# Kernel optimization log

Hardware: AMD Instinct MI355X
Metric: run time of the kernel (lower is better)

## Reference

```python
import jax, jax.numpy as jnp
import numpy as np


def setup_inputs() -> dict:
    key = jax.random.key(0)
    k1, k2 = jax.random.split(key)
    B, Lc, Lm, D = 8, 2048, 2048, 128
    context = jax.random.normal(k1, (B, Lc, D), dtype=jnp.float32)
    main = jax.random.normal(k2, (B, Lm, D), dtype=jnp.float32)
    return {"context": context, "main": main}


def reference(context, main):
    # weights[b,c,m] = sum_d context[b,c,d] * main[b,m,d]   (Keras dot axes=[2,2])
    weights = jnp.einsum("bcd,bmd->bcm", context, main)
    # K.softmax default axis=-1: normalize over the main-length axis m
    weights = jax.nn.softmax(weights, axis=-1)
    # dot([weights, context], axes=1): contract axis 1 (c) of both -> (B, Lm, D)
    weighted = jnp.einsum("bcm,bcd->bmd", weights, context)
    return main - weighted
```

## Files before the change

### kernel.cpp

```cpp
#include <hip/hip_runtime.h>


#define BATCH 8
#define L_SEQ 2048
#define DD 128
#define SHIFT 40.0f
#define LDA 136

typedef __attribute__((ext_vector_type(8))) short bf16x8;
typedef __attribute__((ext_vector_type(4))) short bf16x4;
typedef __attribute__((ext_vector_type(4))) float f32x4;

__device__ __forceinline__ short f2bf(float f) {
    unsigned u = __builtin_bit_cast(unsigned, f);
    return (short)((u + 0x8000u) >> 16);
}

__device__ __forceinline__ void gl2lds16(const short* g, short* l) {
    __builtin_amdgcn_global_load_lds(
        (const __attribute__((address_space(1))) unsigned int*)g,
        (__attribute__((address_space(3))) unsigned int*)l, 16, 0, 0);
}

template <int NT>
__device__ __forceinline__ void stage_tile(short* __restrict__ dst,
                                           const float* __restrict__ src,
                                           int nelts, int t) {
    for (int base = 0; base < nelts; base += NT * 8) {
        int flat = base + t * 8;
        const float4* p = (const float4*)(src + flat);
        float4 v0 = p[0];
        float4 v1 = p[1];
        bf16x8 s;
        s[0] = f2bf(v0.x); s[1] = f2bf(v0.y); s[2] = f2bf(v0.z); s[3] = f2bf(v0.w);
        s[4] = f2bf(v1.x); s[5] = f2bf(v1.y); s[6] = f2bf(v1.z); s[7] = f2bf(v1.w);
        int row = flat >> 7;
        int col = flat & 127;
        *(bf16x8*)&dst[row * LDA + col] = s;
    }
}

__global__ __launch_bounds__(256) void zero_kernel(float* __restrict__ p, int n) {
    int i = blockIdx.x * 256 + threadIdx.x;
    if (i < n) p[i] = 0.0f;
}


__global__ __launch_bounds__(256) void convert_kernel(const float* __restrict__ ctx,
                                                      const float* __restrict__ mn,
                                                      short* __restrict__ Cbf,
                                                      short* __restrict__ Mbf,
                                                      float* __restrict__ Lg) {
    int tid = blockIdx.x * 256 + threadIdx.x;
    if (tid < BATCH * L_SEQ) Lg[tid] = 0.0f;
    const int half = BATCH * L_SEQ * DD / 8;
    int id = tid;
    const float* src;
    short* dst;
    if (id < half) { src = ctx; dst = Cbf; }
    else           { id -= half; src = mn; dst = Mbf; }
    int row = id >> 4;
    int lc = id & 15;
    const float4* p = (const float4*)(src + ((size_t)row << 7) + lc * 8);
    float4 v0 = p[0];
    float4 v1 = p[1];
    bf16x8 s;
    s[0] = f2bf(v0.x); s[1] = f2bf(v0.y); s[2] = f2bf(v0.z); s[3] = f2bf(v0.w);
    s[4] = f2bf(v1.x); s[5] = f2bf(v1.y); s[6] = f2bf(v1.z); s[7] = f2bf(v1.w);
    int pc = (lc & 8) | ((lc ^ row) & 7);
    *(bf16x8*)&dst[((size_t)row << 7) + pc * 8] = s;
}

__global__ __launch_bounds__(256, 2) void stats_kernel(const short* __restrict__ Cbf,
                                                       const short* __restrict__ Mbf,
                                                       float* __restrict__ Lg,
                                                       short* __restrict__ Eg) {
    __shared__ short Cs[128 * 128];
    __shared__ short Ms[2][64 * 128];

    int bid = blockIdx.x;
    int mc = bid & 3;
    int ct = (bid >> 2) & 15;
    int b  = bid >> 6;
    int t = threadIdx.x;
    int w = t >> 6;
    int l = t & 63;
    int a15 = l & 15;
    int q = l >> 4;
    int h = a15 & 7;
    int cw = (w & 1) * 64;
    int mw = (w >> 1) * 32;

    {
        const short* gC = Cbf + ((size_t)(b * L_SEQ + ct * 128)) * DD;
        const short* gM = Mbf + ((size_t)(b * L_SEQ + mc * 512)) * DD;
        #pragma unroll
        for (int ii = 0; ii < 8; ++ii) {
            int inst = w * 8 + ii;
            gl2lds16(gC + inst * 512 + l * 8, Cs + inst * 512);
        }
        #pragma unroll
        for (int ii = 0; ii < 4; ++ii) {
            int inst = w * 4 + ii;
            gl2lds16(gM + inst * 512 + l * 8, Ms[0] + inst * 512);
        }
    }

    __syncthreads();

    {
        const short* gM = Mbf + ((size_t)(b * L_SEQ + mc * 512 + 64)) * DD;
        #pragma unroll
        for (int ii = 0; ii < 4; ++ii) {
            int inst = w * 4 + ii;
            gl2lds16(gM + inst * 512 + l * 8, Ms[1] + inst * 512);
        }
    }

    bf16x8 af[4][4];
    #pragma unroll
    for (int ks = 0; ks < 4; ++ks) {
        int aoff = ((ks * 4 + q) ^ h) * 8;
        #pragma unroll
        for (int i = 0; i < 4; ++i)
            af[ks][i] = *(const bf16x8*)&Cs[(cw + i * 16 + a15) * 128 + aoff];
    }

    float ls[4][4] = {};

    for (int ms = 0; ms < 8; ++ms) {
        int bp = ms & 1;
        if (ms > 0) {
            __syncthreads();
            if (ms < 7) {
                const short* gM = Mbf + ((size_t)(b * L_SEQ + mc * 512 + (ms + 1) * 64)) * DD;
                #pragma unroll
                for (int ii = 0; ii < 4; ++ii) {
                    int inst = w * 4 + ii;
                    gl2lds16(gM + inst * 512 + l * 8, Ms[bp ^ 1] + inst * 512);
                }
            }
        }

        f32x4 acc[4][2];
        #pragma unroll
        for (int i = 0; i < 4; ++i)
            #pragma unroll
            for (int j = 0; j < 2; ++j) {
                f32x4 z = {0.f, 0.f, 0.f, 0.f};
                acc[i][j] = z;
            }
        #pragma unroll
        for (int ks = 0; ks < 4; ++ks) {
            int aoff = ((ks * 4 + q) ^ h) * 8;
            bf16x8 bv[2];
            #pragma unroll
            for (int j = 0; j < 2; ++j)
                bv[j] = *(const bf16x8*)&Ms[bp][(mw + j * 16 + a15) * 128 + aoff];
            #pragma unroll
            for (int i = 0; i < 4; ++i)
                #pragma unroll
                for (int j = 0; j < 2; ++j)
                    acc[i][j] = __builtin_amdgcn_mfma_f32_16x16x32_bf16(af[ks][i], bv[j], acc[i][j], 0, 0, 0);
        }

        #pragma unroll
        for (int j = 0; j < 2; ++j) {
            int m = mc * 512 + ms * 64 + mw + j * 16 + a15;
            size_t rowb = ((size_t)(b * L_SEQ + m)) * L_SEQ;
            #pragma unroll
            for (int i = 0; i < 4; ++i) {
                bf16x4 pk;
                #pragma unroll
                for (int r = 0; r < 4; ++r) {
                    float e = __expf(acc[i][j][r] - SHIFT);
                    ls[i][r] += e;
                    pk[r] = f2bf(e);
                }
                int cq = ct * 128 + cw + i * 16 + q * 4;
                int chunk = cq >> 3;
                int pcc = (chunk & ~7) | ((chunk ^ m) & 7);
                *(bf16x4*)&Eg[rowb + pcc * 8 + (cq & 7)] = pk;
            }
        }
    }

    #pragma unroll
    for (int i = 0; i < 4; ++i)
        #pragma unroll
        for (int r = 0; r < 4; ++r) {
            float v = ls[i][r];
            v += __shfl_xor(v, 1);
            v += __shfl_xor(v, 2);
            v += __shfl_xor(v, 4);
            v += __shfl_xor(v, 8);
            ls[i][r] = v;
        }
    if (a15 == 0) {
        #pragma unroll
        for (int i = 0; i < 4; ++i) {
            int c = ct * 128 + cw + i * 16 + q * 4;
            #pragma unroll
            for (int r = 0; r < 4; ++r)
                atomicAdd(&Lg[(size_t)b * L_SEQ + c + r], ls[i][r]);
        }
    }
}

__global__ __launch_bounds__(256) void prep_kernel(const float* __restrict__ ctx,
                                                   const float* __restrict__ Lg,
                                                   short* __restrict__ CtL) {
    __shared__ short Ts[128 * LDA];
    __shared__ float invLs[128];

    int b = blockIdx.x >> 4;
    int cc = blockIdx.x & 15;
    int t = threadIdx.x;

    if (t < 128) invLs[t] = 1.0f / Lg[(size_t)b * L_SEQ + cc * 128 + t];
    __syncthreads();

    const float* src = ctx + ((size_t)(b * L_SEQ + cc * 128)) * DD;
    #pragma unroll
    for (int i = 0; i < 8; ++i) {
        int flat = i * 2048 + t * 8;
        int r = flat >> 7;
        int c = flat & 127;
        const float4* p = (const float4*)(src + flat);
        float4 v0 = p[0];
        float4 v1 = p[1];
        float il = invLs[r];
        bf16x8 s;
        s[0] = f2bf(v0.x * il); s[1] = f2bf(v0.y * il); s[2] = f2bf(v0.z * il); s[3] = f2bf(v0.w * il);
        s[4] = f2bf(v1.x * il); s[5] = f2bf(v1.y * il); s[6] = f2bf(v1.z * il); s[7] = f2bf(v1.w * il);
        *(bf16x8*)&Ts[r * LDA + c] = s;
    }
    __syncthreads();

    int d = t >> 1;
    int ch = (t & 1) * 64;
    int key = d & 7;
    #pragma unroll
    for (int i = 0; i < 8; ++i) {
        int c = ch + i * 8;
        bf16x8 v;
        #pragma unroll
        for (int j = 0; j < 8; ++j) v[j] = Ts[(c + j) * LDA + d];
        int pc = cc * 16 + (ch >> 3) + (i ^ key);
        *(bf16x8*)&CtL[((size_t)(b * DD + d)) * L_SEQ + pc * 8] = v;
    }
}

__global__ __launch_bounds__(256, 2) void attend_kernel(const short* __restrict__ Eg,
                                                        const short* __restrict__ CtL,
                                                        const float* __restrict__ mn,
                                                        float* __restrict__ out) {
    __shared__ short Et2[2][32 * 128];
    __shared__ short Ct2[2][128 * 128];

    int bid = blockIdx.x;
    int mtile = bid & 63;
    int b = bid >> 6;
    int m0 = mtile * 32;
    int t = threadIdx.x;
    int w = t >> 6;
    int l = t & 63;
    int a15 = l & 15;
    int q = l >> 4;
    int h = a15 & 7;
    int lcc = l & 15;

    f32x4 acc[2][2] = {{{0.f,0.f,0.f,0.f},{0.f,0.f,0.f,0.f}},
                       {{0.f,0.f,0.f,0.f},{0.f,0.f,0.f,0.f}}};

    #pragma unroll
    for (int ii = 0; ii < 2; ++ii) {
        int inst = w * 2 + ii;
        gl2lds16(Eg + ((size_t)(b * L_SEQ + m0 + inst * 4 + q)) * L_SEQ + lcc * 8,
                 &Et2[0][inst * 512]);
    }
    #pragma unroll
    for (int ii = 0; ii < 8; ++ii) {
        int inst = w * 8 + ii;
        gl2lds16(CtL + ((size_t)(b * DD + inst * 4 + q)) * L_SEQ + lcc * 8,
                 &Ct2[0][inst * 512]);
    }

    for (int cs = 0; cs < 16; ++cs) {
        int bp = cs & 1;
        __syncthreads();

        if (cs < 15) {
            int c0 = (cs + 1) * 128;
            #pragma unroll
            for (int ii = 0; ii < 2; ++ii) {
                int inst = w * 2 + ii;
                gl2lds16(Eg + ((size_t)(b * L_SEQ + m0 + inst * 4 + q)) * L_SEQ + c0 + lcc * 8,
                         &Et2[bp ^ 1][inst * 512]);
            }
            #pragma unroll
            for (int ii = 0; ii < 8; ++ii) {
                int inst = w * 8 + ii;
                gl2lds16(CtL + ((size_t)(b * DD + inst * 4 + q)) * L_SEQ + c0 + lcc * 8,
                         &Ct2[bp ^ 1][inst * 512]);
            }
        }

        const short* EtB = Et2[bp];
        const short* CtB = Ct2[bp];
        #pragma unroll
        for (int ks = 0; ks < 4; ++ks) {
            int aoff = ((ks * 4 + q) ^ h) * 8;
            bf16x8 a0 = *(const bf16x8*)&EtB[a15 * 128 + aoff];
            bf16x8 a1 = *(const bf16x8*)&EtB[(16 + a15) * 128 + aoff];
            bf16x8 b0 = *(const bf16x8*)&CtB[((w * 2 + 0) * 16 + a15) * 128 + aoff];
            bf16x8 b1 = *(const bf16x8*)&CtB[((w * 2 + 1) * 16 + a15) * 128 + aoff];
            acc[0][0] = __builtin_amdgcn_mfma_f32_16x16x32_bf16(a0, b0, acc[0][0], 0, 0, 0);
            acc[0][1] = __builtin_amdgcn_mfma_f32_16x16x32_bf16(a0, b1, acc[0][1], 0, 0, 0);
            acc[1][0] = __builtin_amdgcn_mfma_f32_16x16x32_bf16(a1, b0, acc[1][0], 0, 0, 0);
            acc[1][1] = __builtin_amdgcn_mfma_f32_16x16x32_bf16(a1, b1, acc[1][1], 0, 0, 0);
        }
    }

    #pragma unroll
    for (int mg = 0; mg < 2; ++mg) {
        #pragma unroll
        for (int g = 0; g < 2; ++g) {
            int d = (w * 2 + g) * 16 + a15;
            #pragma unroll
            for (int r = 0; r < 4; ++r) {
                int m = m0 + mg * 16 + q * 4 + r;
                size_t idx = ((size_t)(b * L_SEQ + m)) * DD + d;
                out[idx] = mn[idx] - acc[mg][g][r];
            }
        }
    }
}


__global__ __launch_bounds__(256, 4) void stats_fb(const float* __restrict__ ctx,
                                                   const float* __restrict__ mn,
                                                   float* __restrict__ Lg) {
    __shared__ short Cs[64 * LDA];
    __shared__ short Ms[64 * LDA];

    int bid = blockIdx.x;
    int mc = bid & 3;
    int ct = (bid >> 2) & 31;
    int b  = bid >> 7;
    int t = threadIdx.x;
    int w = t >> 6;
    int l = t & 63;
    int a15 = l & 15;
    int q = l >> 4;

    stage_tile<256>(Cs, ctx + ((size_t)b * L_SEQ + ct * 64) * DD, 64 * DD, t);

    float ls[4] = {0.f, 0.f, 0.f, 0.f};
    for (int mt = 0; mt < 8; ++mt) {
        __syncthreads();
        int m0 = (mc * 8 + mt) * 64;
        stage_tile<256>(Ms, mn + ((size_t)b * L_SEQ + m0) * DD, 64 * DD, t);
        __syncthreads();

        f32x4 acc[4] = {{0.f,0.f,0.f,0.f},{0.f,0.f,0.f,0.f},{0.f,0.f,0.f,0.f},{0.f,0.f,0.f,0.f}};
        #pragma unroll
        for (int ks = 0; ks < 4; ++ks) {
            int k0 = ks * 32 + q * 8;
            bf16x8 a = *(const bf16x8*)&Cs[(w * 16 + a15) * LDA + k0];
            #pragma unroll
            for (int g = 0; g < 4; ++g) {
                bf16x8 bb = *(const bf16x8*)&Ms[(g * 16 + a15) * LDA + k0];
                acc[g] = __builtin_amdgcn_mfma_f32_16x16x32_bf16(a, bb, acc[g], 0, 0, 0);
            }
        }
        #pragma unroll
        for (int g = 0; g < 4; ++g)
            #pragma unroll
            for (int r = 0; r < 4; ++r)
                ls[r] += __expf(acc[g][r] - SHIFT);
    }

    #pragma unroll
    for (int r = 0; r < 4; ++r) {
        float v = ls[r];
        v += __shfl_xor(v, 1);
        v += __shfl_xor(v, 2);
        v += __shfl_xor(v, 4);
        v += __shfl_xor(v, 8);
        ls[r] = v;
    }
    if (a15 == 0) {
        int c = ct * 64 + w * 16 + q * 4;
        #pragma unroll
        for (int r = 0; r < 4; ++r)
            atomicAdd(&Lg[(size_t)b * L_SEQ + c + r], ls[r]);
    }
}

__global__ __launch_bounds__(1024, 4) void attend_fb(const float* __restrict__ ctx,
                                                     const float* __restrict__ mn,
                                                     const float* __restrict__ Lg,
                                                     float* __restrict__ out) {
    __shared__ short Mt[64 * LDA];
    __shared__ short Cs[128 * LDA];
    __shared__ short Ct[128 * LDA];
    __shared__ short Ps[64 * LDA];
    __shared__ float invLs[128];

    int bid = blockIdx.x;
    int mtile = bid & 31;
    int b = bid >> 5;
    int m0 = mtile * 64;
    int t = threadIdx.x;
    int w = t >> 6;
    int l = t & 63;
    int a15 = l & 15;
    int q = l >> 4;
    int mg = w & 3;
    int pg = w >> 2;

    stage_tile<1024>(Mt, mn + ((size_t)b * L_SEQ + m0) * DD, 64 * DD, t);

    f32x4 oacc[2] = {{0.f,0.f,0.f,0.f},{0.f,0.f,0.f,0.f}};

    for (int cs = 0; cs < 16; ++cs) {
        int c0 = cs * 128;
        __syncthreads();
        stage_tile<1024>(Cs, ctx + ((size_t)b * L_SEQ + c0) * DD, 128 * DD, t);
        if (t < 128) invLs[t] = 1.0f / Lg[(size_t)b * L_SEQ + c0 + t];
        __syncthreads();

        {
            int cc = t & 127;
            int d0 = (t >> 7) * 16;
            #pragma unroll
            for (int hh = 0; hh < 2; ++hh) {
                bf16x8 v = *(const bf16x8*)&Cs[cc * LDA + d0 + hh * 8];
                #pragma unroll
                for (int j = 0; j < 8; ++j)
                    Ct[(d0 + hh * 8 + j) * LDA + cc] = v[j];
            }
        }

        f32x4 sacc[2] = {{0.f,0.f,0.f,0.f},{0.f,0.f,0.f,0.f}};
        #pragma unroll
        for (int ks = 0; ks < 4; ++ks) {
            int k0 = ks * 32 + q * 8;
            bf16x8 a = *(const bf16x8*)&Mt[(mg * 16 + a15) * LDA + k0];
            #pragma unroll
            for (int g = 0; g < 2; ++g) {
                bf16x8 bb = *(const bf16x8*)&Cs[((pg * 2 + g) * 16 + a15) * LDA + k0];
                sacc[g] = __builtin_amdgcn_mfma_f32_16x16x32_bf16(a, bb, sacc[g], 0, 0, 0);
            }
        }
        #pragma unroll
        for (int g = 0; g < 2; ++g) {
            int cl = (pg * 2 + g) * 16 + a15;
            float il = invLs[cl];
            #pragma unroll
            for (int r = 0; r < 4; ++r) {
                float p = __expf(sacc[g][r] - SHIFT) * il;
                Ps[(mg * 16 + q * 4 + r) * LDA + cl] = f2bf(p);
            }
        }
        __syncthreads();

        #pragma unroll
        for (int ks = 0; ks < 4; ++ks) {
            int k0 = ks * 32 + q * 8;
            bf16x8 a = *(const bf16x8*)&Ps[(mg * 16 + a15) * LDA + k0];
            #pragma unroll
            for (int g = 0; g < 2; ++g) {
                bf16x8 bb = *(const bf16x8*)&Ct[((pg * 2 + g) * 16 + a15) * LDA + k0];
                oacc[g] = __builtin_amdgcn_mfma_f32_16x16x32_bf16(a, bb, oacc[g], 0, 0, 0);
            }
        }
    }

    #pragma unroll
    for (int g = 0; g < 2; ++g) {
        int dl = (pg * 2 + g) * 16 + a15;
        #pragma unroll
        for (int r = 0; r < 4; ++r) {
            int ml = mg * 16 + q * 4 + r;
            size_t idx = ((size_t)b * L_SEQ + m0 + ml) * DD + dl;
            out[idx] = mn[idx] - oacc[g][r];
        }
    }
}


extern "C" void kernel_launch(void* const* d_in, const int* in_sizes, int n_in,
                              void* d_out, int out_size, void* d_ws, size_t ws_size,
                              hipStream_t stream) {
    const float* ctx = (const float*)d_in[0];
    const float* mn  = (const float*)d_in[1];
    float* out = (float*)d_out;

    const size_t LG_BYTES = (size_t)BATCH * L_SEQ * sizeof(float);
    const size_t BF_BYTES = (size_t)BATCH * L_SEQ * DD * sizeof(short);
    const size_t E_BYTES  = (size_t)BATCH * L_SEQ * L_SEQ * sizeof(short);
    const size_t NEED = LG_BYTES + 3 * BF_BYTES + E_BYTES;

    float* Lg = (float*)d_ws;

    if (ws_size >= NEED) {
        short* Cbf = (short*)((char*)d_ws + LG_BYTES);
        short* Mbf = (short*)((char*)d_ws + LG_BYTES + BF_BYTES);
        short* CtL = (short*)((char*)d_ws + LG_BYTES + 2 * BF_BYTES);
        short* Eg  = (short*)((char*)d_ws + LG_BYTES + 3 * BF_BYTES);
        convert_kernel<<<2048, 256, 0, stream>>>(ctx, mn, Cbf, Mbf, Lg);
        stats_kernel<<<BATCH * 16 * 4, 256, 0, stream>>>(Cbf, Mbf, Lg, Eg);
        prep_kernel<<<BATCH * 16, 256, 0, stream>>>(ctx, Lg, CtL);
        attend_kernel<<<BATCH * 64, 256, 0, stream>>>(Eg, CtL, mn, out);
    } else {
        int nL = BATCH * L_SEQ;
        zero_kernel<<<(nL + 255) / 256, 256, 0, stream>>>(Lg, nL);
        stats_fb<<<BATCH * 32 * 4, 256, 0, stream>>>(ctx, mn, Lg);
        attend_fb<<<BATCH * 32, 1024, 0, stream>>>(ctx, mn, Lg, out);
    }
}
```

Baseline: 114.5 us.

## Recompute exp scores in attend kernel instead of materializing E matrix

The stats kernel no longer writes the bf16 exponentiated score matrix (B×L×L) to global memory. A new fused attend kernel recomputes the context·main scores with 32x32 MFMAs, applies exp, repacks the results in registers via lane shuffles into A operands, and accumulates against the normalized transposed context. Partial outputs from the four c-split waves are reduced through LDS. This removes a 64MB write and read of E at the cost of recomputing the first GEMM.

After: 119.2 us. 1.04x slower.

```diff
diff --git a/kernel.cpp b/kernel.cpp
--- a/kernel.cpp
+++ b/kernel.cpp
@@ -10,6 +10,8 @@
 typedef __attribute__((ext_vector_type(8))) short bf16x8;
 typedef __attribute__((ext_vector_type(4))) short bf16x4;
 typedef __attribute__((ext_vector_type(4))) float f32x4;
+typedef __attribute__((ext_vector_type(16))) float f32x16;
+typedef __attribute__((ext_vector_type(4))) unsigned int uint4v;
 
 __device__ __forceinline__ short f2bf(float f) {
     unsigned u = __builtin_bit_cast(unsigned, f);
@@ -73,8 +75,7 @@
 
 __global__ __launch_bounds__(256, 2) void stats_kernel(const short* __restrict__ Cbf,
                                                        const short* __restrict__ Mbf,
-                                                       float* __restrict__ Lg,
-                                                       short* __restrict__ Eg) {
+                                                       float* __restrict__ Lg) {
     __shared__ short Cs[128 * 128];
     __shared__ short Ms[2][64 * 128];
 
@@ -165,24 +166,12 @@
         }
 
         #pragma unroll
-        for (int j = 0; j < 2; ++j) {
-            int m = mc * 512 + ms * 64 + mw + j * 16 + a15;
-            size_t rowb = ((size_t)(b * L_SEQ + m)) * L_SEQ;
-            #pragma unroll
-            for (int i = 0; i < 4; ++i) {
-                bf16x4 pk;
+        for (int j = 0; j < 2; ++j)
+            #pragma unroll
+            for (int i = 0; i < 4; ++i)
                 #pragma unroll
-                for (int r = 0; r < 4; ++r) {
-                    float e = __expf(acc[i][j][r] - SHIFT);
-                    ls[i][r] += e;
-                    pk[r] = f2bf(e);
-                }
-                int cq = ct * 128 + cw + i * 16 + q * 4;
-                int chunk = cq >> 3;
-                int pcc = (chunk & ~7) | ((chunk ^ m) & 7);
-                *(bf16x4*)&Eg[rowb + pcc * 8 + (cq & 7)] = pk;
-            }
-        }
+                for (int r = 0; r < 4; ++r)
+                    ls[i][r] += __expf(acc[i][j][r] - SHIFT);
     }
 
     #pragma unroll
@@ -251,88 +240,164 @@
     }
 }
 
-__global__ __launch_bounds__(256, 2) void attend_kernel(const short* __restrict__ Eg,
-                                                        const short* __restrict__ CtL,
-                                                        const float* __restrict__ mn,
-                                                        float* __restrict__ out) {
-    __shared__ short Et2[2][32 * 128];
-    __shared__ short Ct2[2][128 * 128];
+__global__ __launch_bounds__(512, 2) void attend_fused(const short* __restrict__ Cbf,
+                                                       const short* __restrict__ Mbf,
+                                                       const short* __restrict__ CtL,
+                                                       const float* __restrict__ mn,
+                                                       float* __restrict__ out) {
+    __shared__ __align__(16) char smem[131072];
 
     int bid = blockIdx.x;
-    int mtile = bid & 63;
-    int b = bid >> 6;
-    int m0 = mtile * 32;
+    int mtile = bid & 31;
+    int b = bid >> 5;
     int t = threadIdx.x;
     int w = t >> 6;
     int l = t & 63;
-    int a15 = l & 15;
-    int q = l >> 4;
-    int h = a15 & 7;
-    int lcc = l & 15;
-
-    f32x4 acc[2][2] = {{{0.f,0.f,0.f,0.f},{0.f,0.f,0.f,0.f}},
-                       {{0.f,0.f,0.f,0.f},{0.f,0.f,0.f,0.f}}};
-
-    #pragma unroll
-    for (int ii = 0; ii < 2; ++ii) {
-        int inst = w * 2 + ii;
-        gl2lds16(Eg + ((size_t)(b * L_SEQ + m0 + inst * 4 + q)) * L_SEQ + lcc * 8,
-                 &Et2[0][inst * 512]);
-    }
-    #pragma unroll
-    for (int ii = 0; ii < 8; ++ii) {
-        int inst = w * 8 + ii;
-        gl2lds16(CtL + ((size_t)(b * DD + inst * 4 + q)) * L_SEQ + lcc * 8,
-                 &Ct2[0][inst * 512]);
-    }
+    int la = l & 31;
+    int hi = l >> 5;
+    int mg = w >> 2;
+    int ch = w & 3;
+
+    int m_glob = mtile * 64 + mg * 32 + la;
+
+    bf16x8 mf[8];
+    {
+        const short* mrow = Mbf + ((size_t)(b * L_SEQ + m_glob)) * DD;
+        int key = m_glob & 7;
+        #pragma unroll
+        for (int ks = 0; ks < 8; ++ks) {
+            int lc = ks * 2 + hi;
+            int pc = (lc & 8) | ((lc ^ key) & 7);
+            mf[ks] = *(const bf16x8*)&mrow[pc * 8];
+        }
+    }
+
+    auto stage = [&](int cs, int p) {
+        short* Cw = (short*)(smem + p * 65536);
+        short* Tw = (short*)(smem + p * 65536 + 32768);
+        const short* gC = Cbf + ((size_t)(b * L_SEQ + cs * 128)) * DD;
+        #pragma unroll
+        for (int ii = 0; ii < 4; ++ii) {
+            int inst = w * 4 + ii;
+            gl2lds16(gC + inst * 512 + l * 8, Cw + inst * 512);
+        }
+        const short* gT = CtL + (size_t)b * DD * L_SEQ + (size_t)cs * 128;
+        #pragma unroll
+        for (int ii = 0; ii < 4; ++ii) {
+            int inst = w * 4 + ii;
+            int row = inst * 4 + (l >> 4);
+            gl2lds16(gT + (size_t)row * L_SEQ + (l & 15) * 8, Tw + inst * 512);
+        }
+    };
+
+    f32x16 o[4];
+    #pragma unroll
+    for (int dg = 0; dg < 4; ++dg)
+        #pragma unroll
+        for (int r = 0; r < 16; ++r) o[dg][r] = 0.0f;
+
+    stage(0, 0);
 
     for (int cs = 0; cs < 16; ++cs) {
-        int bp = cs & 1;
+        int p = cs & 1;
         __syncthreads();
-
-        if (cs < 15) {
-            int c0 = (cs + 1) * 128;
-            #pragma unroll
-            for (int ii = 0; ii < 2; ++ii) {
-                int inst = w * 2 + ii;
-                gl2lds16(Eg + ((size_t)(b * L_SEQ + m0 + inst * 4 + q)) * L_SEQ + c0 + lcc * 8,
-                         &Et2[bp ^ 1][inst * 512]);
-            }
-            #pragma unroll
-            for (int ii = 0; ii < 8; ++ii) {
-                int inst = w * 8 + ii;
-                gl2lds16(CtL + ((size_t)(b * DD + inst * 4 + q)) * L_SEQ + c0 + lcc * 8,
-                         &Ct2[bp ^ 1][inst * 512]);
-            }
-        }
-
-        const short* EtB = Et2[bp];
-        const short* CtB = Ct2[bp];
-        #pragma unroll
-        for (int ks = 0; ks < 4; ++ks) {
-            int aoff = ((ks * 4 + q) ^ h) * 8;
-            bf16x8 a0 = *(const bf16x8*)&EtB[a15 * 128 + aoff];
-            bf16x8 a1 = *(const bf16x8*)&EtB[(16 + a15) * 128 + aoff];
-            bf16x8 b0 = *(const bf16x8*)&CtB[((w * 2 + 0) * 16 + a15) * 128 + aoff];
-            bf16x8 b1 = *(const bf16x8*)&CtB[((w * 2 + 1) * 16 + a15) * 128 + aoff];
-            acc[0][0] = __builtin_amdgcn_mfma_f32_16x16x32_bf16(a0, b0, acc[0][0], 0, 0, 0);
-            acc[0][1] = __builtin_amdgcn_mfma_f32_16x16x32_bf16(a0, b1, acc[0][1], 0, 0, 0);
-            acc[1][0] = __builtin_amdgcn_mfma_f32_16x16x32_bf16(a1, b0, acc[1][0], 0, 0, 0);
-            acc[1][1] = __builtin_amdgcn_mfma_f32_16x16x32_bf16(a1, b1, acc[1][1], 0, 0, 0);
-        }
-    }
-
-    #pragma unroll
-    for (int mg = 0; mg < 2; ++mg) {
-        #pragma unroll
-        for (int g = 0; g < 2; ++g) {
-            int d = (w * 2 + g) * 16 + a15;
-            #pragma unroll
-            for (int r = 0; r < 4; ++r) {
-                int m = m0 + mg * 16 + q * 4 + r;
-                size_t idx = ((size_t)(b * L_SEQ + m)) * DD + d;
-                out[idx] = mn[idx] - acc[mg][g][r];
-            }
+        if (cs < 15) stage(cs + 1, p ^ 1);
+
+        const short* Cw = (const short*)(smem + p * 65536);
+        const short* Tw = (const short*)(smem + p * 65536 + 32768);
+
+        f32x16 s;
+        #pragma unroll
+        for (int r = 0; r < 16; ++r) s[r] = 0.0f;
+        int crow = ch * 32 + la;
+        int ckey = la & 7;
+        #pragma unroll
+        for (int ks = 0; ks < 8; ++ks) {
+            int lc = ks * 2 + hi;
+            int pc = (lc & 8) | ((lc ^ ckey) & 7);
+            bf16x8 av = *(const bf16x8*)&Cw[crow * 128 + pc * 8];
+            s = __builtin_amdgcn_mfma_f32_32x32x16_bf16(av, mf[ks], s, 0, 0, 0);
+        }
+
+        unsigned u[4][2];
+        #pragma unroll
+        for (int q = 0; q < 4; ++q)
+            #pragma unroll
+            for (int jj = 0; jj < 2; ++jj) {
+                float e0 = __expf(s[q * 4 + jj * 2]     - SHIFT);
+                float e1 = __expf(s[q * 4 + jj * 2 + 1] - SHIFT);
+                u[q][jj] = ((unsigned)(unsigned short)f2bf(e1) << 16)
+                         |  (unsigned)(unsigned short)f2bf(e0);
+            }
+
+        bf16x8 pa[2];
+        #pragma unroll
+        for (int ks2 = 0; ks2 < 2; ++ks2) {
+            unsigned a0 = u[2 * ks2][0],     a1 = u[2 * ks2][1];
+            unsigned b0 = u[2 * ks2 + 1][0], b1 = u[2 * ks2 + 1][1];
+            unsigned a0p = (unsigned)__shfl_xor((int)a0, 32);
+            unsigned a1p = (unsigned)__shfl_xor((int)a1, 32);
+            unsigned b0p = (unsigned)__shfl_xor((int)b0, 32);
+            unsigned b1p = (unsigned)__shfl_xor((int)b1, 32);
+            uint4v pw;
+            pw.x = hi ? b0p : a0;
+            pw.y = hi ? b1p : a1;
+            pw.z = hi ? b0  : a0p;
+            pw.w = hi ? b1  : a1p;
+            pa[ks2] = __builtin_bit_cast(bf16x8, pw);
+        }
+
+        #pragma unroll
+        for (int dg = 0; dg < 4; ++dg) {
+            int drow = dg * 32 + la;
+            int dkey = drow & 7;
+            #pragma unroll
+            for (int ks2 = 0; ks2 < 2; ++ks2) {
+                int lc2 = ch * 4 + ks2 * 2 + hi;
+                int pc2 = (lc2 & 8) | ((lc2 ^ dkey) & 7);
+                bf16x8 tv = *(const bf16x8*)&Tw[drow * 128 + pc2 * 8];
+                o[dg] = __builtin_amdgcn_mfma_f32_32x32x16_bf16(tv, pa[ks2], o[dg], 0, 0, 0);
+            }
+        }
+    }
+
+    __syncthreads();
+    float* red = (float*)smem;
+    {
+        float* base = red + w * 4096;
+        #pragma unroll
+        for (int dg = 0; dg < 4; ++dg)
+            #pragma unroll
+            for (int r = 0; r < 16; ++r) {
+                int d = dg * 32 + (r & 3) + 8 * (r >> 2) + 4 * hi;
+                base[d * 32 + la] = o[dg][r];
+            }
+    }
+    __syncthreads();
+
+    {
+        int mg2 = t >> 8;
+        int dq  = (t >> 5) & 7;
+        int m   = t & 31;
+        int m_out = mtile * 64 + mg2 * 32 + m;
+        size_t gbase = ((size_t)(b * L_SEQ + m_out)) * DD + dq * 16;
+        const float* r0 = red + (mg2 * 4 + 0) * 4096;
+        const float* r1 = red + (mg2 * 4 + 1) * 4096;
+        const float* r2 = red + (mg2 * 4 + 2) * 4096;
+        const float* r3 = red + (mg2 * 4 + 3) * 4096;
+        #pragma unroll
+        for (int jq = 0; jq < 4; ++jq) {
+            f32x4 v;
+            #pragma unroll
+            for (int e = 0; e < 4; ++e) {
+                int idx = (dq * 16 + jq * 4 + e) * 32 + m;
+                v[e] = r0[idx] + r1[idx] + r2[idx] + r3[idx];
+            }
+            f32x4 mv = *(const f32x4*)&mn[gbase + jq * 4];
+            f32x4 ov;
+            ov[0] = mv[0] - v[0]; ov[1] = mv[1] - v[1];
+            ov[2] = mv[2] - v[2]; ov[3] = mv[3] - v[3];
+            *(f32x4*)&out[gbase + jq * 4] = ov;
         }
     }
 }
@@ -500,8 +565,7 @@
 
     const size_t LG_BYTES = (size_t)BATCH * L_SEQ * sizeof(float);
     const size_t BF_BYTES = (size_t)BATCH * L_SEQ * DD * sizeof(short);
-    const size_t E_BYTES  = (size_t)BATCH * L_SEQ * L_SEQ * sizeof(short);
-    const size_t NEED = LG_BYTES + 3 * BF_BYTES + E_BYTES;
+    const size_t NEED = LG_BYTES + 3 * BF_BYTES;
 
     float* Lg = (float*)d_ws;
 
@@ -509,11 +573,10 @@
         short* Cbf = (short*)((char*)d_ws + LG_BYTES);
         short* Mbf = (short*)((char*)d_ws + LG_BYTES + BF_BYTES);
         short* CtL = (short*)((char*)d_ws + LG_BYTES + 2 * BF_BYTES);
-        short* Eg  = (short*)((char*)d_ws + LG_BYTES + 3 * BF_BYTES);
         convert_kernel<<<2048, 256, 0, stream>>>(ctx, mn, Cbf, Mbf, Lg);
-        stats_kernel<<<BATCH * 16 * 4, 256, 0, stream>>>(Cbf, Mbf, Lg, Eg);
+        stats_kernel<<<BATCH * 16 * 4, 256, 0, stream>>>(Cbf, Mbf, Lg);
         prep_kernel<<<BATCH * 16, 256, 0, stream>>>(ctx, Lg, CtL);
-        attend_kernel<<<BATCH * 64, 256, 0, stream>>>(Eg, CtL, mn, out);
+        attend_fused<<<BATCH * 32, 512, 0, stream>>>(Cbf, Mbf, CtL, mn, out);
     } else {
         int nL = BATCH * L_SEQ;
         zero_kernel<<<(nL + 255) / 256, 256, 0, stream>>>(Lg, nL);
```
